# Performance work log

Hardware: AMD Instinct MI355X
Metric: run time of the kernel (lower is better)

## Reference

```python
import jax, jax.numpy as jnp
import numpy as np

B, S, D = 2, 2048, 1024
N_HEAD, D_ATTN = 16, 64


def setup_inputs() -> dict:
    key = jax.random.key(0)
    ks = jax.random.split(key, 5)
    x = jax.random.normal(ks[0], (B, S, D), dtype=jnp.float32)
    # causal mask: True = masked (as consumed by torch.masked_fill)
    mask = jnp.triu(jnp.ones((S, S), dtype=bool), k=1)
    scale = 0.02
    w_q = jax.random.normal(ks[1], (D, N_HEAD * D_ATTN), dtype=jnp.float32) * scale
    w_k = jax.random.normal(ks[2], (D, N_HEAD * D_ATTN), dtype=jnp.float32) * scale
    w_v = jax.random.normal(ks[3], (D, N_HEAD * D_ATTN), dtype=jnp.float32) * scale
    w_o = jax.random.normal(ks[4], (N_HEAD * D_ATTN, D), dtype=jnp.float32) * scale
    return {"x": x, "mask": mask, "w_q": w_q, "w_k": w_k, "w_v": w_v, "w_o": w_o}


def _split(t):
    # [B,S,H*Da] -> [B,H,S,Da]
    b, s, _ = t.shape
    return t.reshape(b, s, N_HEAD, D_ATTN).transpose(0, 2, 1, 3)


def reference(x, mask, w_q, w_k, w_v, w_o):
    q = _split(x @ w_q)
    k = _split(x @ w_k)
    v = _split(x @ w_v)
    scale = D_ATTN ** 0.5
    score = jnp.einsum("bhqd,bhkd->bhqk", q, k) / scale  # [B,H,S,S]
    score = jnp.where(mask, -jnp.inf, score)
    prob = jax.nn.softmax(score, axis=-1)
    out = jnp.einsum("bhqk,bhkd->bhqd", prob, v)
    out = out.transpose(0, 2, 1, 3).reshape(x.shape[0], x.shape[1], N_HEAD * D_ATTN)
    return out @ w_o
```

## Files before the change

kernel.cpp:

```cpp
#include <hip/hip_runtime.h>
#include <stdint.h>

using u16 = unsigned short;
using u32 = unsigned int;
using u64 = unsigned long long;

typedef float f32x4 __attribute__((ext_vector_type(4)));
typedef __bf16 bf16x8 __attribute__((ext_vector_type(8)));

#define DEV static __device__ __forceinline__

DEV u16 f2bf(float f) {
  u32 u = __float_as_uint(f);
  u += 0x7FFFu + ((u >> 16) & 1u);
  return (u16)(u >> 16);
}

DEV void gld16(const void* g, void* l) {
  __builtin_amdgcn_global_load_lds((__attribute__((address_space(1))) void*)g,
                                   (__attribute__((address_space(3))) void*)l,
                                   16, 0, 0);
}

__global__ void k_cvt(const float* __restrict__ x, u16* __restrict__ xb,
                      const float* __restrict__ w0, const float* __restrict__ w1,
                      const float* __restrict__ w2, const float* __restrict__ w3,
                      u16* __restrict__ t0, u16* __restrict__ t1,
                      u16* __restrict__ t2, u16* __restrict__ t3) {
  const int tid = threadIdx.x;
  if (blockIdx.x < 2048) {
    int i = (blockIdx.x * 256 + tid) * 8;
    float4 a = *(const float4*)&x[i];
    float4 b = *(const float4*)&x[i + 4];
    __align__(16) u16 o[8];
    o[0] = f2bf(a.x); o[1] = f2bf(a.y); o[2] = f2bf(a.z); o[3] = f2bf(a.w);
    o[4] = f2bf(b.x); o[5] = f2bf(b.y); o[6] = f2bf(b.z); o[7] = f2bf(b.w);
    *(uint4*)&xb[i] = *(const uint4*)o;
    return;
  }
  const int c = blockIdx.x - 2048;
  const int z = c >> 8, rem = c & 255;
  const float* w = z == 0 ? w0 : z == 1 ? w1 : z == 2 ? w2 : w3;
  u16* wt       = z == 0 ? t0 : z == 1 ? t1 : z == 2 ? t2 : t3;
  __shared__ __align__(16) float tile[64][68];
  const int k0 = (rem & 15) * 64, n0 = (rem >> 4) * 64;
#pragma unroll
  for (int i = 0; i < 4; ++i) {
    int cc = tid + i * 256;
    int kr = cc >> 4, col = (cc & 15) * 4;
    *(float4*)&tile[kr][col] = *(const float4*)&w[(size_t)(k0 + kr) * 1024 + n0 + col];
  }
  __syncthreads();
#pragma unroll
  for (int i = 0; i < 2; ++i) {
    int cc = tid + i * 256;
    int nr = cc >> 3, kc = (cc & 7) * 8;
    __align__(16) u16 o[8];
#pragma unroll
    for (int j = 0; j < 8; ++j) o[j] = f2bf(tile[kc + j][nr]);
    *(uint4*)&wt[(size_t)(n0 + nr) * 1024 + k0 + kc] = *(const uint4*)o;
  }
}

DEV void gemm_mainloop(const u16* __restrict__ A, const u16* __restrict__ Bt,
                       int m0, int n0, u16* Asb, u16* Bsb, f32x4 (&acc)[4][4]) {
  const int tid = threadIdx.x;
  const int lane = tid & 63;
  const int wv = tid >> 6;
  const int wm = (wv >> 1) * 64, wn = (wv & 1) * 64;

#pragma unroll
  for (int i = 0; i < 4; ++i)
#pragma unroll
    for (int j = 0; j < 4; ++j) {
      f32x4 z = {0.f, 0.f, 0.f, 0.f};
      acc[i][j] = z;
    }

  const int c0 = wv * 64 + lane, c1 = c0 + 256;
  const int r0 = c0 >> 2, r1 = c1 >> 2;
  const int b0 = (c0 & 3) ^ (r0 & 3) ^ ((r0 >> 2) & 3);
  const int b1 = (c1 & 3) ^ (r1 & 3) ^ ((r1 >> 2) & 3);
  const u16* ga0 = A + (size_t)(m0 + r0) * 1024 + b0 * 8;
  const u16* ga1 = A + (size_t)(m0 + r1) * 1024 + b1 * 8;
  const u16* gb0 = Bt + (size_t)(n0 + r0) * 1024 + b0 * 8;
  const u16* gb1 = Bt + (size_t)(n0 + r1) * 1024 + b1 * 8;
  const int da0 = (wv * 64) * 8, da1 = (wv * 64 + 256) * 8;

  int aoff[4], boff[4];
#pragma unroll
  for (int f = 0; f < 4; ++f) {
    int ra = wm + f * 16 + (lane & 15);
    aoff[f] = ra * 32 + (((lane >> 4) ^ (ra & 3) ^ ((ra >> 2) & 3)) * 8);
    int rb = wn + f * 16 + (lane & 15);
    boff[f] = rb * 32 + (((lane >> 4) ^ (rb & 3) ^ ((rb >> 2) & 3)) * 8);
  }

#pragma unroll
  for (int p = 0; p < 2; ++p) {
    const int k0 = p * 32, bo = p * 4096;
    gld16(ga0 + k0, Asb + bo + da0);
    gld16(ga1 + k0, Asb + bo + da1);
    gld16(gb0 + k0, Bsb + bo + da0);
    gld16(gb1 + k0, Bsb + bo + da1);
  }

#pragma unroll 1
  for (int kt = 0; kt < 32; ++kt) {
    if (kt < 31) asm volatile("s_waitcnt vmcnt(4)" ::: "memory");
    else         asm volatile("s_waitcnt vmcnt(0)" ::: "memory");
    __builtin_amdgcn_s_barrier();
    __builtin_amdgcn_sched_barrier(0);

    if (kt + 2 < 32) {
      const int k0 = (kt + 2) * 32, bo = ((kt + 2) % 3) * 4096;
      gld16(ga0 + k0, Asb + bo + da0);
      gld16(ga1 + k0, Asb + bo + da1);
      gld16(gb0 + k0, Bsb + bo + da0);
      gld16(gb1 + k0, Bsb + bo + da1);
    }

    const int bo = (kt % 3) * 4096;
    bf16x8 af[4], bfv[4];
#pragma unroll
    for (int f = 0; f < 4; ++f) af[f] = *(const bf16x8*)&Asb[bo + aoff[f]];
#pragma unroll
    for (int f = 0; f < 4; ++f) bfv[f] = *(const bf16x8*)&Bsb[bo + boff[f]];
#pragma unroll
    for (int i = 0; i < 4; ++i)
#pragma unroll
      for (int j = 0; j < 4; ++j)
        acc[i][j] = __builtin_amdgcn_mfma_f32_16x16x32_bf16(af[i], bfv[j], acc[i][j], 0, 0, 0);
  }
}

__global__ __launch_bounds__(256) void k_gemm_qkv(
    const u16* __restrict__ X, const u16* __restrict__ Wq, const u16* __restrict__ Wk,
    const u16* __restrict__ Wv, u16* __restrict__ Q, u16* __restrict__ K,
    u16* __restrict__ V) {
  __shared__ __align__(16) u16 Asb[3 * 4096];
  __shared__ __align__(16) u16 Bsb[3 * 4096];
  const int nb = blockIdx.x, mb = blockIdx.y;
  const int proj = nb >> 3, n0 = (nb & 7) * 128;
  const u16* W = proj == 0 ? Wq : proj == 1 ? Wk : Wv;
  u16* Dst = proj == 0 ? Q : proj == 1 ? K : V;
  const float scl = proj == 0 ? 0.125f * 1.4426950408889634f : 1.0f;
  f32x4 acc[4][4];
  gemm_mainloop(X, W, mb * 128, n0, Asb, Bsb, acc);
  const int lane = threadIdx.x & 63, wv = threadIdx.x >> 6;
  const int wm = (wv >> 1) * 64, wn = (wv & 1) * 64;
#pragma unroll
  for (int i = 0; i < 4; ++i)
#pragma unroll
    for (int j = 0; j < 4; ++j)
#pragma unroll
      for (int r = 0; r < 4; ++r) {
        int m = mb * 128 + wm + i * 16 + (lane >> 4) * 4 + r;
        int n = n0 + wn + j * 16 + (lane & 15);
        int b = m >> 11, s = m & 2047, h = n >> 6, d = n & 63;
        Dst[(size_t)((b * 16 + h) * 2048 + s) * 64 + d] = f2bf(acc[i][j][r] * scl);
      }
}

__global__ __launch_bounds__(256) void k_gemm_out(
    const u16* __restrict__ A, const u16* __restrict__ Wt, float* __restrict__ Out) {
  __shared__ __align__(16) u16 Asb[3 * 4096];
  __shared__ __align__(16) u16 Bsb[3 * 4096];
  const int nb = blockIdx.x, mb = blockIdx.y;
  f32x4 acc[4][4];
  gemm_mainloop(A, Wt, mb * 128, nb * 128, Asb, Bsb, acc);
  const int lane = threadIdx.x & 63, wv = threadIdx.x >> 6;
  const int wm = (wv >> 1) * 64, wn = (wv & 1) * 64;
#pragma unroll
  for (int i = 0; i < 4; ++i)
#pragma unroll
    for (int j = 0; j < 4; ++j)
#pragma unroll
      for (int r = 0; r < 4; ++r) {
        int m = mb * 128 + wm + i * 16 + (lane >> 4) * 4 + r;
        int n = nb * 128 + wn + j * 16 + (lane & 15);
        Out[(size_t)m * 1024 + n] = acc[i][j][r];
      }
}

__global__ void k_transpose_v(const u16* __restrict__ V, u16* __restrict__ Vt) {
  __shared__ __align__(16) u16 t[64][80];
  const int bh = blockIdx.y, s0 = blockIdx.x * 64;
  const int tid = threadIdx.x;
#pragma unroll
  for (int i = 0; i < 2; ++i) {
    int c = tid + i * 256;
    int sr = c >> 3, dc = (c & 7) * 8;
    *(uint4*)&t[sr][dc] = *(const uint4*)&V[((size_t)bh * 2048 + s0 + sr) * 64 + dc];
  }
  __syncthreads();
#pragma unroll
  for (int i = 0; i < 2; ++i) {
    int c = tid + i * 256;
    int dr = c >> 3, c7 = c & 7;
    __align__(8) u16 o[8];
#pragma unroll
    for (int j = 0; j < 8; ++j) o[j] = t[c7 * 8 + j][dr];
    int bp = ((c7 >> 1) & 1) * 32 + (c7 & 1) * 16 + ((c7 >> 2) & 1) * 4;
    u16* row = &Vt[((size_t)bh * 64 + dr) * 2048 + s0];
    *(u64*)&row[bp]     = *(const u64*)&o[0];
    *(u64*)&row[bp + 8] = *(const u64*)&o[4];
  }
}

DEV void qk_tile(const u16* Kc, const bf16x8 (&qf)[2], int lo, int hi, f32x4 (&sc)[4]) {
#pragma unroll
  for (int cf = 0; cf < 4; ++cf) {
    f32x4 z = {0.f, 0.f, 0.f, 0.f};
    sc[cf] = z;
#pragma unroll
    for (int kf = 0; kf < 2; ++kf) {
      int row = cf * 16 + lo;
      int blk = ((kf * 4 + hi) ^ (row & 7)) * 8;
      bf16x8 kfr = *(const bf16x8*)&Kc[row * 64 + blk];
      sc[cf] = __builtin_amdgcn_mfma_f32_16x16x32_bf16(kfr, qf[kf], sc[cf], 0, 0, 0);
    }
  }
}

DEV void sm_pv(f32x4 (&sc)[4], const u16* Vc, int lane, int lo, int hi,
               float& m_run, float& l_run, f32x4 (&ao)[4]) {
  float mx0 = fmaxf(fmaxf(sc[0][0], sc[0][1]), fmaxf(sc[0][2], sc[0][3]));
  float mx1 = fmaxf(fmaxf(sc[1][0], sc[1][1]), fmaxf(sc[1][2], sc[1][3]));
  float mx2 = fmaxf(fmaxf(sc[2][0], sc[2][1]), fmaxf(sc[2][2], sc[2][3]));
  float mx3 = fmaxf(fmaxf(sc[3][0], sc[3][1]), fmaxf(sc[3][2], sc[3][3]));
  float mx = fmaxf(fmaxf(mx0, mx1), fmaxf(mx2, mx3));
  mx = fmaxf(mx, __shfl_xor(mx, 16));
  mx = fmaxf(mx, __shfl_xor(mx, 32));

  if (__any(mx > m_run + 8.0f)) {
    float mnew = fmaxf(m_run, mx);
    float sclf = __builtin_amdgcn_exp2f(m_run - mnew);
    const int base = lane & 48;
#pragma unroll
    for (int r = 0; r < 4; ++r) {
      float s_r = __shfl(sclf, base + hi * 4 + r);
#pragma unroll
      for (int df = 0; df < 4; ++df) ao[df][r] *= s_r;
    }
    l_run *= sclf;
    m_run = mnew;
  }

  float pp[4];
  bf16x8 pa0, pa1;
#pragma unroll
  for (int cf = 0; cf < 4; ++cf) {
    float p0 = __builtin_amdgcn_exp2f(sc[cf][0] - m_run);
    float p1 = __builtin_amdgcn_exp2f(sc[cf][1] - m_run);
    float p2 = __builtin_amdgcn_exp2f(sc[cf][2] - m_run);
    float p3 = __builtin_amdgcn_exp2f(sc[cf][3] - m_run);
    pp[cf] = (p0 + p1) + (p2 + p3);
    bf16x8& pa = (cf & 1) ? pa1 : pa0;
    int j = (cf >> 1) * 4;
    pa[j] = (__bf16)p0; pa[j + 1] = (__bf16)p1;
    pa[j + 2] = (__bf16)p2; pa[j + 3] = (__bf16)p3;
  }
  float psum = (pp[0] + pp[1]) + (pp[2] + pp[3]);
  psum += __shfl_xor(psum, 16);
  psum += __shfl_xor(psum, 32);
  l_run += psum;

  __builtin_amdgcn_s_setprio(1);
#pragma unroll
  for (int df = 0; df < 4; ++df) {
#pragma unroll
    for (int kf = 0; kf < 2; ++kf) {
      int row = df * 16 + lo;
      int blk = ((kf * 4 + hi) ^ (row & 7)) * 8;
      bf16x8 vfr = *(const bf16x8*)&Vc[row * 64 + blk];
      ao[df] = __builtin_amdgcn_mfma_f32_16x16x32_bf16(kf == 0 ? pa0 : pa1, vfr,
                                                       ao[df], 0, 0, 0);
    }
  }
  __builtin_amdgcn_s_setprio(0);
}

__global__ __launch_bounds__(512) void k_attn(
    const u16* __restrict__ Qg, const u16* __restrict__ Kg,
    const u16* __restrict__ Vtg, u16* __restrict__ Og) {
  __shared__ __align__(16) u16 Ks[4][64 * 64];
  __shared__ __align__(16) u16 Vs[4][64 * 64];
  const int tid = threadIdx.x, lane = tid & 63, wv = tid >> 6;
  const int lo = lane & 15, hi = lane >> 4;
  const int w4 = wv & 3, qsel = wv >> 2;

  const int flat = blockIdx.y * 16 + blockIdx.x;
  const int xcd = flat & 7, slot = flat >> 3;
  const int bh = xcd * 4 + (slot >> 4);
  const int jp = slot & 15;

  const u16* Qb = Qg + (size_t)bh * 2048 * 64;
  const u16* Kb = Kg + (size_t)bh * 2048 * 64;
  const u16* Vb = Vtg + (size_t)bh * 64 * 2048;
  const int b = bh >> 4, h = bh & 15;

  const int nta = jp + 1, ntb = 32 - jp;
  const int q0 = (qsel ? (31 - jp) : jp) * 64;
  const int myNt = qsel ? ntb : nta;
  const int qq = q0 + w4 * 16 + lo;

  bf16x8 qf[2];
#pragma unroll
  for (int kf = 0; kf < 2; ++kf)
    qf[kf] = *(const bf16x8*)&Qb[(size_t)(q0 + w4 * 16 + lo) * 64 + kf * 32 + hi * 8];

  f32x4 ao[4];
#pragma unroll
  for (int df = 0; df < 4; ++df) {
    f32x4 z = {0.f, 0.f, 0.f, 0.f};
    ao[df] = z;
  }
  float m_run = -1e30f, l_run = 0.f;

  const int r0 = tid >> 3;
  const int e0 = ((tid & 7) ^ (r0 & 7)) * 8;

#pragma unroll
  for (int p = 0; p < 3; ++p) {
    gld16(Kb + (size_t)(p * 64 + r0) * 64 + e0, &Ks[p][wv * 512]);
    gld16(Vb + (size_t)r0 * 2048 + p * 64 + e0, &Vs[p][wv * 512]);
  }

#pragma unroll 1
  for (int t = 0; t < ntb; ++t) {
    if (t + 2 < ntb)      asm volatile("s_waitcnt vmcnt(4)" ::: "memory");
    else if (t + 1 < ntb) asm volatile("s_waitcnt vmcnt(2)" ::: "memory");
    else                  asm volatile("s_waitcnt vmcnt(0)" ::: "memory");
    __builtin_amdgcn_s_barrier();
    __builtin_amdgcn_sched_barrier(0);

    if (t + 3 < ntb) {
      const int kn = (t + 3) * 64;
      gld16(Kb + (size_t)(kn + r0) * 64 + e0, &Ks[(t + 3) & 3][wv * 512]);
      gld16(Vb + (size_t)r0 * 2048 + kn + e0, &Vs[(t + 3) & 3][wv * 512]);
    }

    if (t < myNt) {
      const u16* Kc = Ks[t & 3];
      const u16* Vc = Vs[t & 3];
      f32x4 sc[4];
      __builtin_amdgcn_s_setprio(1);
      qk_tile(Kc, qf, lo, hi, sc);
      __builtin_amdgcn_s_setprio(0);

      if (t == myNt - 1) {
        const int kv0 = t * 64;
#pragma unroll
        for (int cf = 0; cf < 4; ++cf)
#pragma unroll
          for (int r = 0; r < 4; ++r) {
            int kk = kv0 + cf * 16 + hi * 4 + r;
            if (kk > qq) sc[cf][r] = -1e30f;
          }
      }

      sm_pv(sc, Vc, lane, lo, hi, m_run, l_run, ao);
    }
  }

  float linv[4];
  const int base = lane & 48;
#pragma unroll
  for (int r = 0; r < 4; ++r) {
    float l_r = __shfl(l_run, base + hi * 4 + r);
    linv[r] = 1.0f / l_r;
  }
#pragma unroll
  for (int df = 0; df < 4; ++df)
#pragma unroll
    for (int r = 0; r < 4; ++r) {
      int s = q0 + w4 * 16 + hi * 4 + r;
      int d = df * 16 + lo;
      Og[((size_t)(b * 2048 + s)) * 1024 + h * 64 + d] = f2bf(ao[df][r] * linv[r]);
    }
}

extern "C" void kernel_launch(void* const* d_in, const int* in_sizes, int n_in,
                              void* d_out, int out_size, void* d_ws, size_t ws_size,
                              hipStream_t stream) {
  const float* x = (const float*)d_in[0];
  const float* wq = (const float*)d_in[2];
  const float* wk = (const float*)d_in[3];
  const float* wv = (const float*)d_in[4];
  const float* wo = (const float*)d_in[5];

  char* ws = (char*)d_ws;
  u16* xb  = (u16*)(ws);
  u16* wqt = (u16*)(ws + 8388608);
  u16* wkt = (u16*)(ws + 8388608 + 2097152);
  u16* wvt = (u16*)(ws + 8388608 + 2 * 2097152);
  u16* wot = (u16*)(ws + 8388608 + 3 * 2097152);
  u16* qb  = (u16*)(ws + 16777216);
  u16* kb  = (u16*)(ws + 16777216 + 8388608);
  u16* vb  = (u16*)(ws + 16777216 + 2 * 8388608);
  u16* vt  = (u16*)(ws + 16777216 + 3 * 8388608);
  u16* ao  = (u16*)(ws + 16777216 + 4 * 8388608);

  k_cvt<<<dim3(3072), dim3(256), 0, stream>>>(x, xb, wq, wk, wv, wo, wqt, wkt, wvt, wot);
  k_gemm_qkv<<<dim3(24, 32), dim3(256), 0, stream>>>(xb, wqt, wkt, wvt, qb, kb, vb);
  k_transpose_v<<<dim3(32, 32), dim3(256), 0, stream>>>(vb, vt);
  k_attn<<<dim3(16, 32), dim3(512), 0, stream>>>(qb, kb, vt, ao);
  k_gemm_out<<<dim3(8, 32), dim3(256), 0, stream>>>(ao, wot, (float*)d_out);
}
```

Baseline: 118.9 us.

## Process KV tiles in pairs per iteration with one softmax rescale per pair

Restructures the causal attention main loop so each iteration handles two 64-key tiles. The two QK products run back to back, there is one online-softmax max reduction and rescale per pair, and one barrier per pair. Prefetch now fetches the next pair with a full vmcnt(0) wait, in place of the rolling three-tile-ahead pipeline. The block-to-query-pair mapping is also reversed for half the heads to change load ordering across XCD slots. In exchange, odd tile counts compute a fully masked extra tile, the last tile can be read past the end of a head's K/V rows, and load/compute overlap is shallower.

```diff
diff --git a/kernel.cpp b/kernel.cpp
--- a/kernel.cpp
+++ b/kernel.cpp
@@ -223,64 +223,6 @@
   }
 }
 
-DEV void sm_pv(f32x4 (&sc)[4], const u16* Vc, int lane, int lo, int hi,
-               float& m_run, float& l_run, f32x4 (&ao)[4]) {
-  float mx0 = fmaxf(fmaxf(sc[0][0], sc[0][1]), fmaxf(sc[0][2], sc[0][3]));
-  float mx1 = fmaxf(fmaxf(sc[1][0], sc[1][1]), fmaxf(sc[1][2], sc[1][3]));
-  float mx2 = fmaxf(fmaxf(sc[2][0], sc[2][1]), fmaxf(sc[2][2], sc[2][3]));
-  float mx3 = fmaxf(fmaxf(sc[3][0], sc[3][1]), fmaxf(sc[3][2], sc[3][3]));
-  float mx = fmaxf(fmaxf(mx0, mx1), fmaxf(mx2, mx3));
-  mx = fmaxf(mx, __shfl_xor(mx, 16));
-  mx = fmaxf(mx, __shfl_xor(mx, 32));
-
-  if (__any(mx > m_run + 8.0f)) {
-    float mnew = fmaxf(m_run, mx);
-    float sclf = __builtin_amdgcn_exp2f(m_run - mnew);
-    const int base = lane & 48;
-#pragma unroll
-    for (int r = 0; r < 4; ++r) {
-      float s_r = __shfl(sclf, base + hi * 4 + r);
-#pragma unroll
-      for (int df = 0; df < 4; ++df) ao[df][r] *= s_r;
-    }
-    l_run *= sclf;
-    m_run = mnew;
-  }
-
-  float pp[4];
-  bf16x8 pa0, pa1;
-#pragma unroll
-  for (int cf = 0; cf < 4; ++cf) {
-    float p0 = __builtin_amdgcn_exp2f(sc[cf][0] - m_run);
-    float p1 = __builtin_amdgcn_exp2f(sc[cf][1] - m_run);
-    float p2 = __builtin_amdgcn_exp2f(sc[cf][2] - m_run);
-    float p3 = __builtin_amdgcn_exp2f(sc[cf][3] - m_run);
-    pp[cf] = (p0 + p1) + (p2 + p3);
-    bf16x8& pa = (cf & 1) ? pa1 : pa0;
-    int j = (cf >> 1) * 4;
-    pa[j] = (__bf16)p0; pa[j + 1] = (__bf16)p1;
-    pa[j + 2] = (__bf16)p2; pa[j + 3] = (__bf16)p3;
-  }
-  float psum = (pp[0] + pp[1]) + (pp[2] + pp[3]);
-  psum += __shfl_xor(psum, 16);
-  psum += __shfl_xor(psum, 32);
-  l_run += psum;
-
-  __builtin_amdgcn_s_setprio(1);
-#pragma unroll
-  for (int df = 0; df < 4; ++df) {
-#pragma unroll
-    for (int kf = 0; kf < 2; ++kf) {
-      int row = df * 16 + lo;
-      int blk = ((kf * 4 + hi) ^ (row & 7)) * 8;
-      bf16x8 vfr = *(const bf16x8*)&Vc[row * 64 + blk];
-      ao[df] = __builtin_amdgcn_mfma_f32_16x16x32_bf16(kf == 0 ? pa0 : pa1, vfr,
-                                                       ao[df], 0, 0, 0);
-    }
-  }
-  __builtin_amdgcn_s_setprio(0);
-}
-
 __global__ __launch_bounds__(512) void k_attn(
     const u16* __restrict__ Qg, const u16* __restrict__ Kg,
     const u16* __restrict__ Vtg, u16* __restrict__ Og) {
@@ -292,8 +234,9 @@
 
   const int flat = blockIdx.y * 16 + blockIdx.x;
   const int xcd = flat & 7, slot = flat >> 3;
-  const int bh = xcd * 4 + (slot >> 4);
-  const int jp = slot & 15;
+  const int q4 = slot >> 4, r = slot & 15;
+  const int bh = xcd * 4 + q4;
+  const int jp = (q4 & 2) ? (15 - r) : r;
 
   const u16* Qb = Qg + (size_t)bh * 2048 * 64;
   const u16* Kb = Kg + (size_t)bh * 2048 * 64;
@@ -303,6 +246,8 @@
   const int nta = jp + 1, ntb = 32 - jp;
   const int q0 = (qsel ? (31 - jp) : jp) * 64;
   const int myNt = qsel ? ntb : nta;
+  const int myU = (myNt + 1) >> 1;
+  const int ub = (ntb + 1) >> 1;
   const int qq = q0 + w4 * 16 + lo;
 
   bf16x8 qf[2];
@@ -322,62 +267,125 @@
   const int e0 = ((tid & 7) ^ (r0 & 7)) * 8;
 
 #pragma unroll
-  for (int p = 0; p < 3; ++p) {
+  for (int p = 0; p < 2; ++p) {
     gld16(Kb + (size_t)(p * 64 + r0) * 64 + e0, &Ks[p][wv * 512]);
     gld16(Vb + (size_t)r0 * 2048 + p * 64 + e0, &Vs[p][wv * 512]);
   }
 
 #pragma unroll 1
-  for (int t = 0; t < ntb; ++t) {
-    if (t + 2 < ntb)      asm volatile("s_waitcnt vmcnt(4)" ::: "memory");
-    else if (t + 1 < ntb) asm volatile("s_waitcnt vmcnt(2)" ::: "memory");
-    else                  asm volatile("s_waitcnt vmcnt(0)" ::: "memory");
+  for (int u = 0; u < ub; ++u) {
+    asm volatile("s_waitcnt vmcnt(0)" ::: "memory");
     __builtin_amdgcn_s_barrier();
     __builtin_amdgcn_sched_barrier(0);
 
-    if (t + 3 < ntb) {
-      const int kn = (t + 3) * 64;
-      gld16(Kb + (size_t)(kn + r0) * 64 + e0, &Ks[(t + 3) & 3][wv * 512]);
-      gld16(Vb + (size_t)r0 * 2048 + kn + e0, &Vs[(t + 3) & 3][wv * 512]);
-    }
-
-    if (t < myNt) {
-      const u16* Kc = Ks[t & 3];
-      const u16* Vc = Vs[t & 3];
-      f32x4 sc[4];
+    if (u + 1 < ub) {
+      const int bb = 2 * u + 2;
+#pragma unroll
+      for (int p = 0; p < 2; ++p) {
+        const int bi = bb + p;
+        gld16(Kb + (size_t)(bi * 64 + r0) * 64 + e0, &Ks[bi & 3][wv * 512]);
+        gld16(Vb + (size_t)r0 * 2048 + bi * 64 + e0, &Vs[bi & 3][wv * 512]);
+      }
+    }
+
+    if (u < myU) {
+      f32x4 sc[2][4];
       __builtin_amdgcn_s_setprio(1);
-      qk_tile(Kc, qf, lo, hi, sc);
+      qk_tile(Ks[(2 * u) & 3], qf, lo, hi, sc[0]);
+      qk_tile(Ks[(2 * u + 1) & 3], qf, lo, hi, sc[1]);
       __builtin_amdgcn_s_setprio(0);
 
-      if (t == myNt - 1) {
-        const int kv0 = t * 64;
-#pragma unroll
-        for (int cf = 0; cf < 4; ++cf)
-#pragma unroll
-          for (int r = 0; r < 4; ++r) {
-            int kk = kv0 + cf * 16 + hi * 4 + r;
-            if (kk > qq) sc[cf][r] = -1e30f;
+      if (u == myU - 1) {
+#pragma unroll
+        for (int h2 = 0; h2 < 2; ++h2)
+#pragma unroll
+          for (int cf = 0; cf < 4; ++cf)
+#pragma unroll
+            for (int rr = 0; rr < 4; ++rr) {
+              int kk = u * 128 + h2 * 64 + cf * 16 + hi * 4 + rr;
+              if (kk > qq) sc[h2][cf][rr] = -1e30f;
+            }
+      }
+
+      float mx = sc[0][0][0];
+#pragma unroll
+      for (int h2 = 0; h2 < 2; ++h2)
+#pragma unroll
+        for (int cf = 0; cf < 4; ++cf) {
+          mx = fmaxf(mx, fmaxf(fmaxf(sc[h2][cf][0], sc[h2][cf][1]),
+                               fmaxf(sc[h2][cf][2], sc[h2][cf][3])));
+        }
+      mx = fmaxf(mx, __shfl_xor(mx, 16));
+      mx = fmaxf(mx, __shfl_xor(mx, 32));
+
+      if (__any(mx > m_run + 8.0f)) {
+        float mnew = fmaxf(m_run, mx);
+        float sclf = __builtin_amdgcn_exp2f(m_run - mnew);
+        const int base = lane & 48;
+#pragma unroll
+        for (int rr = 0; rr < 4; ++rr) {
+          float s_r = __shfl(sclf, base + hi * 4 + rr);
+#pragma unroll
+          for (int df = 0; df < 4; ++df) ao[df][rr] *= s_r;
+        }
+        l_run *= sclf;
+        m_run = mnew;
+      }
+
+      float pptot = 0.f;
+#pragma unroll
+      for (int h2 = 0; h2 < 2; ++h2) {
+        const u16* Vc = Vs[(2 * u + h2) & 3];
+        bf16x8 pa0, pa1;
+        float pp[4];
+#pragma unroll
+        for (int cf = 0; cf < 4; ++cf) {
+          float p0 = __builtin_amdgcn_exp2f(sc[h2][cf][0] - m_run);
+          float p1 = __builtin_amdgcn_exp2f(sc[h2][cf][1] - m_run);
+          float p2 = __builtin_amdgcn_exp2f(sc[h2][cf][2] - m_run);
+          float p3 = __builtin_amdgcn_exp2f(sc[h2][cf][3] - m_run);
+          pp[cf] = (p0 + p1) + (p2 + p3);
+          bf16x8& pa = (cf & 1) ? pa1 : pa0;
+          int j = (cf >> 1) * 4;
+          pa[j] = (__bf16)p0; pa[j + 1] = (__bf16)p1;
+          pa[j + 2] = (__bf16)p2; pa[j + 3] = (__bf16)p3;
+        }
+        pptot += (pp[0] + pp[1]) + (pp[2] + pp[3]);
+        __builtin_amdgcn_s_setprio(1);
+#pragma unroll
+        for (int df = 0; df < 4; ++df) {
+#pragma unroll
+          for (int kf = 0; kf < 2; ++kf) {
+            int row = df * 16 + lo;
+            int blk = ((kf * 4 + hi) ^ (row & 7)) * 8;
+            bf16x8 vfr = *(const bf16x8*)&Vc[row * 64 + blk];
+            ao[df] = __builtin_amdgcn_mfma_f32_16x16x32_bf16(kf == 0 ? pa0 : pa1, vfr,
+                                                             ao[df], 0, 0, 0);
           }
-      }
-
-      sm_pv(sc, Vc, lane, lo, hi, m_run, l_run, ao);
+        }
+        __builtin_amdgcn_s_setprio(0);
+      }
+      float psum = pptot;
+      psum += __shfl_xor(psum, 16);
+      psum += __shfl_xor(psum, 32);
+      l_run += psum;
     }
   }
 
   float linv[4];
   const int base = lane & 48;
 #pragma unroll
-  for (int r = 0; r < 4; ++r) {
-    float l_r = __shfl(l_run, base + hi * 4 + r);
-    linv[r] = 1.0f / l_r;
+  for (int rr = 0; rr < 4; ++rr) {
+    float l_r = __shfl(l_run, base + hi * 4 + rr);
+    linv[rr] = 1.0f / l_r;
   }
 #pragma unroll
   for (int df = 0; df < 4; ++df)
 #pragma unroll
-    for (int r = 0; r < 4; ++r) {
-      int s = q0 + w4 * 16 + hi * 4 + r;
+    for (int rr = 0; rr < 4; ++rr) {
+      int s = q0 + w4 * 16 + hi * 4 + rr;
       int d = df * 16 + lo;
-      Og[((size_t)(b * 2048 + s)) * 1024 + h * 64 + d] = f2bf(ao[df][r] * linv[r]);
+      Og[((size_t)(b * 2048 + s)) * 1024 + h * 64 + d] = f2bf(ao[df][rr] * linv[rr]);
     }
 }
 
```

New measurement: 129.1 us. +8.5%, slower.
